# Performance work log

Measured on AMD Instinct MI355X. Metric: run time of the kernel, lower is better.

Reference implementation:

```python
import jax, jax.numpy as jnp
import numpy as np

GRID_SIZE = 64
THRESHOLD = 1.0
SIGMA = 1.5
K_SHARP = 2.0


def _gaussian_kernel(sigma):
    ksize = max(int(4 * sigma) | 1, 3)
    x = jnp.arange(ksize, dtype=jnp.float32) - ksize // 2
    g1d = jnp.exp(-x ** 2 / (2.0 * sigma ** 2))
    g2d = g1d[None, :] * g1d[:, None]
    g2d = g2d / g2d.sum()
    return g2d[None, None]  # (1,1,k,k) OIHW


def setup_inputs() -> dict:
    key = jax.random.key(0)
    k1, k2, k3, k4 = jax.random.split(key, 4)
    B, V, P, N, MAXP = 4, 512, 8192, 2000, 8
    positions = jax.random.uniform(k1, (B, V, 2), dtype=jnp.float32) * 2.0 - 1.0
    pin_offsets = jax.random.normal(k2, (P, 2), dtype=jnp.float32) * 0.05
    net_to_pin = jax.random.randint(k3, (N, MAXP), 0, P, dtype=jnp.int32)
    pin_to_macro = jax.random.randint(k4, (P,), 0, V, dtype=jnp.int32)
    return {"positions": positions, "pin_offsets": pin_offsets,
            "net_to_pin": net_to_pin, "pin_to_macro": pin_to_macro}


def reference(positions, pin_offsets, net_to_pin, pin_to_macro):
    B = positions.shape[0]
    M = GRID_SIZE
    num_nets = net_to_pin.shape[0]

    # pin positions: (B, P, 2) -- no rotation (rotation_onehot=None branch)
    pin_pos = positions[:, pin_to_macro, :] + pin_offsets[None]

    # per-net bounding boxes over valid pins
    valid = net_to_pin >= 0                                  # (N, maxp)
    safe_idx = jnp.maximum(net_to_pin, 0)
    net_pin_pos = pin_pos[:, safe_idx, :]                    # (B, N, maxp, 2)
    mask = valid[None, :, :, None]
    bbox_max = jnp.max(jnp.where(mask, net_pin_pos, -1e9), axis=2)  # (B, N, 2)
    bbox_min = jnp.min(jnp.where(mask, net_pin_pos, 1e9), axis=2)

    # to grid coordinates
    bbox_max_g = (bbox_max + 1.0) * 0.5 * (M - 1)
    bbox_min_g = (bbox_min + 1.0) * 0.5 * (M - 1)

    # soft rectangular indicators on the MxM grid
    gx = jnp.arange(M, dtype=jnp.float32)
    grid_x, grid_y = jnp.meshgrid(gx, gx, indexing="xy")     # (M, M)
    grid_x = grid_x[None, None]                               # (1,1,M,M)
    grid_y = grid_y[None, None]
    x_min = bbox_min_g[..., 0][..., None, None]               # (B,N,1,1)
    x_max = bbox_max_g[..., 0][..., None, None]
    y_min = bbox_min_g[..., 1][..., None, None]
    y_max = bbox_max_g[..., 1][..., None, None]

    in_x = jax.nn.sigmoid(K_SHARP * (grid_x - x_min + 0.5)) * \
           jax.nn.sigmoid(K_SHARP * (x_max - grid_x + 0.5))
    in_y = jax.nn.sigmoid(K_SHARP * (grid_y - y_min + 0.5)) * \
           jax.nn.sigmoid(K_SHARP * (y_max - grid_y + 0.5))
    indicator = in_x * in_y                                    # (B,N,M,M)

    bbox_size = jnp.maximum((x_max - x_min + 1.0) * (y_max - y_min + 1.0), 1.0)
    rudy = jnp.sum(indicator / bbox_size, axis=1, keepdims=True)  # (B,1,M,M)

    # gaussian smoothing (SAME padding)
    kernel = _gaussian_kernel(SIGMA)
    pad = kernel.shape[-1] // 2
    rudy_smooth = jax.lax.conv_general_dilated(
        rudy, kernel, window_strides=(1, 1),
        padding=((pad, pad), (pad, pad)),
        dimension_numbers=("NCHW", "OIHW", "NCHW"))

    overflow = jax.nn.relu(rudy_smooth - THRESHOLD)
    penalty = jnp.sum(overflow ** 2, axis=(1, 2, 3))           # (B,)
    return penalty, rudy_smooth
```

## Files before the change

### kernel.cpp

```cpp
#include <hip/hip_runtime.h>

#define GRID   64
#define BATCH  4
#define NV     512
#define NP     8192
#define NNET   2000
#define MAXPIN 8
#define NB     32
#define NCHUNK 63

__device__ __forceinline__ float sigmoidf_fast(float z) {
    return 1.0f / (1.0f + __expf(-z));
}

__global__ __launch_bounds__(256)
void rudy_accum_kernel(const float* __restrict__ positions,
                       const float* __restrict__ pin_offsets,
                       const int*   __restrict__ net_to_pin,
                       const int*   __restrict__ pin_to_macro,
                       float* __restrict__ rudy) {
    const int chunk = blockIdx.x;
    const int b     = blockIdx.y;
    const int t     = threadIdx.x;

    __shared__ float s_inx[NB][GRID];
    __shared__ float s_iny[NB][GRID];
    __shared__ float s_xmin[NB], s_xmax[NB], s_ymin[NB], s_ymax[NB], s_inv[NB];

    {
        const int nl = t >> 3;
        const int j  = t & 7;
        const int n  = chunk * NB + nl;
        int pi = (n < NNET) ? net_to_pin[n * MAXPIN + j] : -1;
        int sp = pi > 0 ? pi : 0;
        int v  = pin_to_macro[sp];
        float px = positions[(b * NV + v) * 2 + 0] + pin_offsets[sp * 2 + 0];
        float py = positions[(b * NV + v) * 2 + 1] + pin_offsets[sp * 2 + 1];
        bool valid = pi >= 0;
        float xmx = valid ? px : -1e9f;
        float xmn = valid ? px :  1e9f;
        float ymx = valid ? py : -1e9f;
        float ymn = valid ? py :  1e9f;
        #pragma unroll
        for (int off = 1; off < 8; off <<= 1) {
            xmx = fmaxf(xmx, __shfl_xor(xmx, off, 64));
            xmn = fminf(xmn, __shfl_xor(xmn, off, 64));
            ymx = fmaxf(ymx, __shfl_xor(ymx, off, 64));
            ymn = fminf(ymn, __shfl_xor(ymn, off, 64));
        }
        if (j == 0) {
            float xming = (xmn + 1.0f) * 31.5f;
            float xmaxg = (xmx + 1.0f) * 31.5f;
            float yming = (ymn + 1.0f) * 31.5f;
            float ymaxg = (ymx + 1.0f) * 31.5f;
            float size = fmaxf((xmaxg - xming + 1.0f) * (ymaxg - yming + 1.0f), 1.0f);
            s_xmin[nl] = xming; s_xmax[nl] = xmaxg;
            s_ymin[nl] = yming; s_ymax[nl] = ymaxg;
            s_inv[nl]  = 1.0f / size;
        }
    }
    __syncthreads();

    #pragma unroll
    for (int i = 0; i < 16; ++i) {
        int v     = i * 256 + t;
        int n     = v >> 7;
        int rem   = v & 127;
        int which = rem >> 6;
        int coord = rem & 63;
        float c  = (float)coord;
        float lo = which ? s_ymin[n] : s_xmin[n];
        float hi = which ? s_ymax[n] : s_xmax[n];
        float val = sigmoidf_fast(2.0f * (c - lo + 0.5f)) *
                    sigmoidf_fast(2.0f * (hi - c + 0.5f));
        if (which) s_iny[n][coord] = val; else s_inx[n][coord] = val;
    }
    __syncthreads();

    const int lane = t & 63;
    const int w    = t >> 6;
    float acc[16];
    #pragma unroll
    for (int k = 0; k < 16; ++k) acc[k] = 0.0f;

    for (int n = 0; n < NB; ++n) {
        float xv = s_inx[n][lane] * s_inv[n];
        const float4* iny4 = (const float4*)&s_iny[n][w * 16];
        #pragma unroll
        for (int k4 = 0; k4 < 4; ++k4) {
            float4 yv = iny4[k4];
            acc[k4 * 4 + 0] += yv.x * xv;
            acc[k4 * 4 + 1] += yv.y * xv;
            acc[k4 * 4 + 2] += yv.z * xv;
            acc[k4 * 4 + 3] += yv.w * xv;
        }
    }

    float* dst = rudy + b * (GRID * GRID);
    #pragma unroll
    for (int k = 0; k < 16; ++k) {
        int cell = (w * 16 + k) * GRID + lane;
        atomicAdd(&dst[cell], acc[k]);
    }
}

__global__ __launch_bounds__(256)
void smooth_penalty_kernel(const float* __restrict__ rudy,
                           float* __restrict__ out_penalty,
                           float* __restrict__ out_smooth) {
    const int b = blockIdx.x;
    const int t = threadIdx.x;

    __shared__ float tile[GRID * GRID];
    __shared__ float tmp [GRID * GRID];
    __shared__ float red[4];

    float g[7];
    {
        float s = 0.0f;
        #pragma unroll
        for (int i = 0; i < 7; ++i) {
            float d = (float)(i - 3);
            g[i] = expf(-d * d / 4.5f);
            s += g[i];
        }
        float inv = 1.0f / s;
        #pragma unroll
        for (int i = 0; i < 7; ++i) g[i] *= inv;
    }

    const float* src = rudy + b * GRID * GRID;
    #pragma unroll
    for (int k = 0; k < 16; ++k) tile[k * 256 + t] = src[k * 256 + t];
    __syncthreads();

    #pragma unroll
    for (int k = 0; k < 16; ++k) {
        int c = k * 256 + t;
        int y = c >> 6, x = c & 63;
        float s = 0.0f;
        #pragma unroll
        for (int d = -3; d <= 3; ++d) {
            int xx = x + d;
            if (xx >= 0 && xx < GRID) s += g[d + 3] * tile[y * GRID + xx];
        }
        tmp[c] = s;
    }
    __syncthreads();

    float local = 0.0f;
    #pragma unroll
    for (int k = 0; k < 16; ++k) {
        int c = k * 256 + t;
        int y = c >> 6, x = c & 63;
        float s = 0.0f;
        #pragma unroll
        for (int d = -3; d <= 3; ++d) {
            int yy = y + d;
            if (yy >= 0 && yy < GRID) s += g[d + 3] * tmp[yy * GRID + x];
        }
        out_smooth[b * GRID * GRID + c] = s;
        float ov = s - 1.0f;
        ov = ov > 0.0f ? ov : 0.0f;
        local += ov * ov;
    }

    #pragma unroll
    for (int off = 32; off > 0; off >>= 1) local += __shfl_down(local, off, 64);
    if ((t & 63) == 0) red[t >> 6] = local;
    __syncthreads();
    if (t == 0) out_penalty[b] = red[0] + red[1] + red[2] + red[3];
}

extern "C" void kernel_launch(void* const* d_in, const int* in_sizes, int n_in,
                              void* d_out, int out_size, void* d_ws, size_t ws_size,
                              hipStream_t stream) {
    const float* positions    = (const float*)d_in[0];
    const float* pin_offsets  = (const float*)d_in[1];
    const int*   net_to_pin   = (const int*)d_in[2];
    const int*   pin_to_macro = (const int*)d_in[3];
    float* out  = (float*)d_out;
    float* rudy = (float*)d_ws;

    hipMemsetAsync(d_ws, 0, BATCH * GRID * GRID * sizeof(float), stream);
    rudy_accum_kernel<<<dim3(NCHUNK, BATCH), 256, 0, stream>>>(
        positions, pin_offsets, net_to_pin, pin_to_macro, rudy);
    smooth_penalty_kernel<<<BATCH, 256, 0, stream>>>(rudy, out, out + BATCH);
}
```

Before: 76.65 us.

## Replace atomic accumulation with per-chunk partials reduced in smoothing kernel

Each accumulation block now writes its 64x64 partial grid to its own workspace slice instead of doing float atomicAdds into a shared grid. The smoothing kernel, widened to 1024 threads, sums the 63 partials per batch before the separable Gaussian and penalty reduction. This removes the memset and atomic contention, and the run-to-run ordering nondeterminism that came with the atomics. In exchange it adds about 4 MB of partial writes and reads, and the final reduction runs on only 4 blocks.

```diff
diff --git a/kernel.cpp b/kernel.cpp
--- a/kernel.cpp
+++ b/kernel.cpp
@@ -8,17 +8,18 @@
 #define MAXPIN 8
 #define NB     32
 #define NCHUNK 63
+#define CELLS  (GRID * GRID)
 
 __device__ __forceinline__ float sigmoidf_fast(float z) {
     return 1.0f / (1.0f + __expf(-z));
 }
 
 __global__ __launch_bounds__(256)
-void rudy_accum_kernel(const float* __restrict__ positions,
-                       const float* __restrict__ pin_offsets,
-                       const int*   __restrict__ net_to_pin,
-                       const int*   __restrict__ pin_to_macro,
-                       float* __restrict__ rudy) {
+void rudy_partial_kernel(const float* __restrict__ positions,
+                         const float* __restrict__ pin_offsets,
+                         const int*   __restrict__ net_to_pin,
+                         const int*   __restrict__ pin_to_macro,
+                         float* __restrict__ partial) {
     const int chunk = blockIdx.x;
     const int b     = blockIdx.y;
     const int t     = threadIdx.x;
@@ -96,24 +97,23 @@
         }
     }
 
-    float* dst = rudy + b * (GRID * GRID);
+    float* dst = partial + (b * NCHUNK + chunk) * CELLS;
     #pragma unroll
     for (int k = 0; k < 16; ++k) {
-        int cell = (w * 16 + k) * GRID + lane;
-        atomicAdd(&dst[cell], acc[k]);
+        dst[(w * 16 + k) * GRID + lane] = acc[k];
     }
 }
 
-__global__ __launch_bounds__(256)
-void smooth_penalty_kernel(const float* __restrict__ rudy,
+__global__ __launch_bounds__(1024)
+void smooth_penalty_kernel(const float* __restrict__ partial,
                            float* __restrict__ out_penalty,
                            float* __restrict__ out_smooth) {
     const int b = blockIdx.x;
     const int t = threadIdx.x;
 
-    __shared__ float tile[GRID * GRID];
-    __shared__ float tmp [GRID * GRID];
-    __shared__ float red[4];
+    __shared__ float tile[CELLS];
+    __shared__ float tmp [CELLS];
+    __shared__ float red[16];
 
     float g[7];
     {
@@ -129,14 +129,20 @@
         for (int i = 0; i < 7; ++i) g[i] *= inv;
     }
 
-    const float* src = rudy + b * GRID * GRID;
+    const float* base = partial + b * NCHUNK * CELLS;
+    float sum[4] = {0.0f, 0.0f, 0.0f, 0.0f};
+    for (int ch = 0; ch < NCHUNK; ++ch) {
+        const float* p = base + ch * CELLS;
+        #pragma unroll
+        for (int k = 0; k < 4; ++k) sum[k] += p[k * 1024 + t];
+    }
     #pragma unroll
-    for (int k = 0; k < 16; ++k) tile[k * 256 + t] = src[k * 256 + t];
+    for (int k = 0; k < 4; ++k) tile[k * 1024 + t] = sum[k];
     __syncthreads();
 
     #pragma unroll
-    for (int k = 0; k < 16; ++k) {
-        int c = k * 256 + t;
+    for (int k = 0; k < 4; ++k) {
+        int c = k * 1024 + t;
         int y = c >> 6, x = c & 63;
         float s = 0.0f;
         #pragma unroll
@@ -150,8 +156,8 @@
 
     float local = 0.0f;
     #pragma unroll
-    for (int k = 0; k < 16; ++k) {
-        int c = k * 256 + t;
+    for (int k = 0; k < 4; ++k) {
+        int c = k * 1024 + t;
         int y = c >> 6, x = c & 63;
         float s = 0.0f;
         #pragma unroll
@@ -159,7 +165,7 @@
             int yy = y + d;
             if (yy >= 0 && yy < GRID) s += g[d + 3] * tmp[yy * GRID + x];
         }
-        out_smooth[b * GRID * GRID + c] = s;
+        out_smooth[b * CELLS + c] = s;
         float ov = s - 1.0f;
         ov = ov > 0.0f ? ov : 0.0f;
         local += ov * ov;
@@ -169,7 +175,12 @@
     for (int off = 32; off > 0; off >>= 1) local += __shfl_down(local, off, 64);
     if ((t & 63) == 0) red[t >> 6] = local;
     __syncthreads();
-    if (t == 0) out_penalty[b] = red[0] + red[1] + red[2] + red[3];
+    if (t == 0) {
+        float s = 0.0f;
+        #pragma unroll
+        for (int i = 0; i < 16; ++i) s += red[i];
+        out_penalty[b] = s;
+    }
 }
 
 extern "C" void kernel_launch(void* const* d_in, const int* in_sizes, int n_in,
@@ -179,11 +190,10 @@
     const float* pin_offsets  = (const float*)d_in[1];
     const int*   net_to_pin   = (const int*)d_in[2];
     const int*   pin_to_macro = (const int*)d_in[3];
-    float* out  = (float*)d_out;
-    float* rudy = (float*)d_ws;
+    float* out     = (float*)d_out;
+    float* partial = (float*)d_ws;
 
-    hipMemsetAsync(d_ws, 0, BATCH * GRID * GRID * sizeof(float), stream);
-    rudy_accum_kernel<<<dim3(NCHUNK, BATCH), 256, 0, stream>>>(
-        positions, pin_offsets, net_to_pin, pin_to_macro, rudy);
-    smooth_penalty_kernel<<<BATCH, 256, 0, stream>>>(rudy, out, out + BATCH);
+    rudy_partial_kernel<<<dim3(NCHUNK, BATCH), 256, 0, stream>>>(
+        positions, pin_offsets, net_to_pin, pin_to_macro, partial);
+    smooth_penalty_kernel<<<BATCH, 1024, 0, stream>>>(partial, out, out + BATCH);
 }
```

Measured after the change: 81.95 us. +6.9%, slower.

## Fuse smoothing and penalty into accumulation kernel via last-block atomic counter

Applied to the files above, without the earlier changes.

Merges the two kernels into one. Each batch gets an atomic completion counter, and the last block to finish accumulating for that batch runs the Gaussian smoothing and the penalty reduction. This removes a kernel launch and the gap between launches. Shared memory grows to 32KB so it can be reused for the smoothing tile, which may lower occupancy of the accumulation phase. The rudy tile load is also vectorized to float4.

```diff
diff --git a/kernel.cpp b/kernel.cpp
--- a/kernel.cpp
+++ b/kernel.cpp
@@ -8,24 +8,31 @@
 #define MAXPIN 8
 #define NB     32
 #define NCHUNK 63
+#define CELLS  (GRID * GRID)
 
 __device__ __forceinline__ float sigmoidf_fast(float z) {
     return 1.0f / (1.0f + __expf(-z));
 }
 
 __global__ __launch_bounds__(256)
-void rudy_accum_kernel(const float* __restrict__ positions,
+void rudy_fused_kernel(const float* __restrict__ positions,
                        const float* __restrict__ pin_offsets,
                        const int*   __restrict__ net_to_pin,
                        const int*   __restrict__ pin_to_macro,
-                       float* __restrict__ rudy) {
+                       float*        __restrict__ rudy,
+                       unsigned int* __restrict__ counters,
+                       float* __restrict__ out_penalty,
+                       float* __restrict__ out_smooth) {
     const int chunk = blockIdx.x;
     const int b     = blockIdx.y;
     const int t     = threadIdx.x;
 
-    __shared__ float s_inx[NB][GRID];
-    __shared__ float s_iny[NB][GRID];
+    __shared__ float smem[2 * CELLS];
+    float* s_inx = smem;
+    float* s_iny = smem + NB * GRID;
     __shared__ float s_xmin[NB], s_xmax[NB], s_ymin[NB], s_ymax[NB], s_inv[NB];
+    __shared__ int   s_last;
+    __shared__ float red[4];
 
     {
         const int nl = t >> 3;
@@ -73,7 +80,7 @@
         float hi = which ? s_ymax[n] : s_xmax[n];
         float val = sigmoidf_fast(2.0f * (c - lo + 0.5f)) *
                     sigmoidf_fast(2.0f * (hi - c + 0.5f));
-        if (which) s_iny[n][coord] = val; else s_inx[n][coord] = val;
+        if (which) s_iny[n * GRID + coord] = val; else s_inx[n * GRID + coord] = val;
     }
     __syncthreads();
 
@@ -84,8 +91,8 @@
     for (int k = 0; k < 16; ++k) acc[k] = 0.0f;
 
     for (int n = 0; n < NB; ++n) {
-        float xv = s_inx[n][lane] * s_inv[n];
-        const float4* iny4 = (const float4*)&s_iny[n][w * 16];
+        float xv = s_inx[n * GRID + lane] * s_inv[n];
+        const float4* iny4 = (const float4*)&s_iny[n * GRID + w * 16];
         #pragma unroll
         for (int k4 = 0; k4 < 4; ++k4) {
             float4 yv = iny4[k4];
@@ -96,24 +103,28 @@
         }
     }
 
-    float* dst = rudy + b * (GRID * GRID);
+    float* dst = rudy + b * CELLS;
     #pragma unroll
     for (int k = 0; k < 16; ++k) {
-        int cell = (w * 16 + k) * GRID + lane;
-        atomicAdd(&dst[cell], acc[k]);
+        atomicAdd(&dst[(w * 16 + k) * GRID + lane], acc[k]);
     }
-}
 
-__global__ __launch_bounds__(256)
-void smooth_penalty_kernel(const float* __restrict__ rudy,
-                           float* __restrict__ out_penalty,
-                           float* __restrict__ out_smooth) {
-    const int b = blockIdx.x;
-    const int t = threadIdx.x;
+    __threadfence();
+    if (t == 0) {
+        unsigned int old = atomicAdd(&counters[b], 1u);
+        s_last = (old == NCHUNK - 1) ? 1 : 0;
+    }
+    __syncthreads();
+    if (!s_last) return;
+    __threadfence();
 
-    __shared__ float tile[GRID * GRID];
-    __shared__ float tmp [GRID * GRID];
-    __shared__ float red[4];
+    float* tile = smem;
+    float* tmp  = smem + CELLS;
+
+    const float4* src4  = (const float4*)(rudy + b * CELLS);
+    float4*       tile4 = (float4*)tile;
+    #pragma unroll
+    for (int k = 0; k < 4; ++k) tile4[k * 256 + t] = src4[k * 256 + t];
 
     float g[7];
     {
@@ -128,10 +139,6 @@
         #pragma unroll
         for (int i = 0; i < 7; ++i) g[i] *= inv;
     }
-
-    const float* src = rudy + b * GRID * GRID;
-    #pragma unroll
-    for (int k = 0; k < 16; ++k) tile[k * 256 + t] = src[k * 256 + t];
     __syncthreads();
 
     #pragma unroll
@@ -159,7 +166,7 @@
             int yy = y + d;
             if (yy >= 0 && yy < GRID) s += g[d + 3] * tmp[yy * GRID + x];
         }
-        out_smooth[b * GRID * GRID + c] = s;
+        out_smooth[b * CELLS + c] = s;
         float ov = s - 1.0f;
         ov = ov > 0.0f ? ov : 0.0f;
         local += ov * ov;
@@ -180,10 +187,11 @@
     const int*   net_to_pin   = (const int*)d_in[2];
     const int*   pin_to_macro = (const int*)d_in[3];
     float* out  = (float*)d_out;
-    float* rudy = (float*)d_ws;
+    float*        rudy     = (float*)d_ws;
+    unsigned int* counters = (unsigned int*)((char*)d_ws + BATCH * CELLS * sizeof(float));
 
-    hipMemsetAsync(d_ws, 0, BATCH * GRID * GRID * sizeof(float), stream);
-    rudy_accum_kernel<<<dim3(NCHUNK, BATCH), 256, 0, stream>>>(
-        positions, pin_offsets, net_to_pin, pin_to_macro, rudy);
-    smooth_penalty_kernel<<<BATCH, 256, 0, stream>>>(rudy, out, out + BATCH);
+    hipMemsetAsync(d_ws, 0, BATCH * CELLS * sizeof(float) + BATCH * sizeof(unsigned int), stream);
+    rudy_fused_kernel<<<dim3(NCHUNK, BATCH), 256, 0, stream>>>(
+        positions, pin_offsets, net_to_pin, pin_to_macro,
+        rudy, counters, out, out + BATCH);
 }
```

Measured after the change: 88.58 us. 15.6% more time.
